# Optimization experiments

Hardware: AMD Instinct MI355X
Metric: run time of the kernel (lower is better)

## Reference

```python
import jax, jax.numpy as jnp
import numpy as np

THR = 1.0   # snntorch Leaky default threshold
BETA = 0.9  # leak factor from the module


@jax.custom_vjp
def atan_spike(x):
    # Heaviside forward; ATan surrogate gradient (snntorch default alpha=2):
    # d/dx = 1 / (1 + (pi * x)^2)
    return (x > 0).astype(x.dtype)

def _atan_fwd(x):
    return (x > 0).astype(x.dtype), x

def _atan_bwd(x, g):
    return (g / (1.0 + (jnp.pi * x) ** 2),)

atan_spike.defvjp(_atan_fwd, _atan_bwd)


def setup_inputs() -> dict:
    key = jax.random.key(0)
    k0, k1, k2, k3, k4 = jax.random.split(key, 5)
    B, T, L = 256, 1000, 30  # 24 = L - 7 + 1 matches fc1 in_features 16*24
    out_c = 35
    x = jax.random.normal(k0, (B, T, L), dtype=jnp.float32)
    conv_w = jax.random.normal(k1, (16, 1, 7), dtype=jnp.float32) / np.float32(np.sqrt(7.0))
    conv_b = jax.random.normal(k2, (16,), dtype=jnp.float32) * 0.05
    fc_w = jax.random.normal(k3, (out_c, 16 * 24), dtype=jnp.float32) / np.float32(np.sqrt(384.0))
    fc_b = jax.random.normal(k4, (out_c,), dtype=jnp.float32) * 0.05
    return {"x": x, "conv_w": conv_w, "conv_b": conv_b, "fc_w": fc_w, "fc_b": fc_b}


def reference(x, conv_w, conv_b, fc_w, fc_b):
    B, T, L = x.shape
    # Conv1d has no recurrence -> hoist it out of the time loop, batched over B*T.
    cur1 = jax.lax.conv_general_dilated(
        x.reshape(B * T, 1, L), conv_w, window_strides=(1,), padding="VALID",
        dimension_numbers=("NCH", "OIH", "NCH"),
    ) + conv_b[None, :, None]                      # (B*T, 16, 24)
    Lo = cur1.shape[-1]
    cur1 = cur1.reshape(B, T, 16, Lo).transpose(1, 0, 2, 3)  # (T, B, 16, 24)
    out_c = fc_w.shape[0]

    def step(carry, c1):
        mem1, mem2 = carry
        # LIF1: reset-by-subtraction using detached spike of previous membrane
        r1 = jax.lax.stop_gradient((mem1 > THR).astype(mem1.dtype))
        mem1 = BETA * mem1 + c1 - r1 * THR
        spk1 = atan_spike(mem1 - THR)              # (B, 16, 24)
        c2 = spk1.reshape(B, 16 * Lo) @ fc_w.T + fc_b  # (B, out_c)
        # LIF2
        r2 = jax.lax.stop_gradient((mem2 > THR).astype(mem2.dtype))
        mem2 = BETA * mem2 + c2 - r2 * THR
        return (mem1, mem2), mem2

    init = (jnp.zeros((B, 16, Lo), x.dtype), jnp.zeros((B, out_c), x.dtype))
    _, mem2_rec = jax.lax.scan(step, init, cur1)   # (T, B, out_c)
    return mem2_rec.mean(axis=0)                   # (B, out_c)
```

## Files before the change

kernel.cpp:

```cpp
#include <hip/hip_runtime.h>

typedef _Float16 half8 __attribute__((ext_vector_type(8)));
typedef float f32x4 __attribute__((ext_vector_type(4)));

#define SPH  32
#define NIT  34
#define SPKW 392
#define XTW  36
#define C2W  48
#define TN   1000

__global__ __launch_bounds__(576, 1) void snn_fwd(
    const float* __restrict__ x,
    const float* __restrict__ conv_w,
    const float* __restrict__ conv_b,
    const float* __restrict__ fc_w,
    const float* __restrict__ fc_b,
    float* __restrict__ out)
{
    __shared__ __align__(16) _Float16 spk[2][SPH][SPKW];
    __shared__ __align__(16) float    xsT[2][30][XTW];
    __shared__ __align__(16) float    c2L[2][SPH][C2W];

    const int tid  = threadIdx.x;
    const int b    = blockIdx.x;
    const int wid  = tid >> 6;
    const int lane = tid & 63;

    const int ct    = tid;
    const int cpair = ct & 7;
    const int p     = ct >> 3;
    const int c0    = cpair * 2;
    float wk0[7], wk1[7];
    float cb0 = 0.f, cb1 = 0.f;
    if (wid < 3) {
#pragma unroll
        for (int k = 0; k < 7; ++k) {
            wk0[k] = conv_w[c0 * 7 + k];
            wk1[k] = conv_w[(c0 + 1) * 7 + k];
        }
        cb0 = conv_b[c0];
        cb1 = conv_b[c0 + 1];
    }

    const int g  = wid - 3;
    const int m  = g >> 1;
    const int tb = g & 1;
    const int nL = lane & 15;
    const int q  = lane >> 4;
    half8 A[12];
    if (wid >= 3) {
        const int o = m * 16 + nL;
#pragma unroll
        for (int kt = 0; kt < 12; ++kt) {
            half8 a;
#pragma unroll
            for (int j = 0; j < 8; ++j) {
                int Kp = kt * 32 + q * 8 + j;
                int Kc = Kp & 15;
                int Kq = Kp >> 4;
                a[j] = (o < 35) ? (_Float16)fc_w[o * 384 + Kc * 24 + Kq]
                                : (_Float16)0.f;
            }
            A[kt] = a;
        }
    }
    const float fcb = (wid == 3 && lane < 35) ? fc_b[lane] : 0.f;

    const int st = tid - 192;
    int fs[3], fl[3];
    if (wid >= 3) {
#pragma unroll
        for (int r = 0; r < 3; ++r) {
            int f = st + 384 * r;
            fs[r] = f / 30;
            fl[r] = f % 30;
        }
    }

    float m1a = 0.f, spa = 0.f;
    float m1b = 0.f, spb = 0.f;
    float mem2 = 0.f, accO = 0.f;
    float xr[3];

    const float* xb = x + (size_t)b * (TN * 30);

    if (wid >= 3) {
#pragma unroll
        for (int r = 0; r < 3; ++r) {
            int f = st + 384 * r;
            if (f < 960) xsT[0][fl[r]][fs[r]] = xb[f];
        }
#pragma unroll
        for (int r = 0; r < 3; ++r) {
            int f = st + 384 * r;
            xr[r] = (f < 960) ? xb[960 + f] : 0.f;
        }
    }
    __syncthreads();

#pragma unroll 1
    for (int ph = 0; ph < NIT; ++ph) {
        if (wid < 3) {
            if (ph < 32) {
                const float* xcol = &xsT[ph & 1][p][0];
                unsigned int* sdst =
                    (unsigned int*)&spk[ph & 1][0][p * 16 + c0];
#pragma unroll 2
                for (int s0 = 0; s0 < SPH; s0 += 4) {
                    f32x4 xv[7];
#pragma unroll
                    for (int k = 0; k < 7; ++k)
                        xv[k] = *(const f32x4*)(xcol + k * XTW + s0);
                    float ca[4], cc[4];
#pragma unroll
                    for (int dt = 0; dt < 4; ++dt) { ca[dt] = cb0; cc[dt] = cb1; }
#pragma unroll
                    for (int k = 0; k < 7; ++k) {
#pragma unroll
                        for (int dt = 0; dt < 4; ++dt) {
                            ca[dt] = fmaf(wk0[k], xv[k][dt], ca[dt]);
                            cc[dt] = fmaf(wk1[k], xv[k][dt], cc[dt]);
                        }
                    }
#pragma unroll
                    for (int dt = 0; dt < 4; ++dt) {
                        m1a = fmaf(0.9f, m1a, ca[dt] - spa);
                        spa = (m1a > 1.0f) ? 1.0f : 0.0f;
                        m1b = fmaf(0.9f, m1b, cc[dt] - spb);
                        spb = (m1b > 1.0f) ? 1.0f : 0.0f;
                        unsigned int pk = (m1a > 1.0f ? 0x00003C00u : 0u) |
                                          (m1b > 1.0f ? 0x3C000000u : 0u);
                        sdst[(s0 + dt) * (SPKW / 2)] = pk;
                    }
                }
            }
        } else {
            const bool ldg = (ph <= 29);
            float xn[3];
            if (ldg) {
                const float* src = xb + (size_t)(ph + 2) * (SPH * 30);
#pragma unroll
                for (int r = 0; r < 3; ++r) {
                    int f = st + 384 * r;
                    int t = (ph + 2) * SPH + fs[r];
                    xn[r] = (f < 960 && t < TN) ? src[f] : 0.f;
                }
            }
            if (ph >= 1 && ph <= 32) {
                const _Float16* sb = &spk[(ph - 1) & 1][0][0];
                half8 B[12];
#pragma unroll
                for (int kt = 0; kt < 12; ++kt)
                    B[kt] = *(const half8*)(sb + (tb * 16 + nL) * SPKW + kt * 32 + q * 8);
                f32x4 acc = {0.f, 0.f, 0.f, 0.f};
#pragma unroll
                for (int kt = 0; kt < 12; ++kt)
                    acc = __builtin_amdgcn_mfma_f32_16x16x32_f16(A[kt], B[kt], acc, 0, 0, 0);
                float* cd = &c2L[(ph - 1) & 1][0][0];
                *(f32x4*)(cd + (tb * 16 + nL) * C2W + m * 16 + q * 4) = acc;
            }
            if (wid == 3 && lane < 35 && ph >= 2) {
                const float* cs = &c2L[(ph - 2) & 1][0][0];
                float v[SPH];
#pragma unroll
                for (int j = 0; j < SPH; ++j) v[j] = cs[j * C2W + lane];
                const int tbase = (ph - 2) * SPH;
#pragma unroll
                for (int j = 0; j < SPH; ++j) {
                    float r2 = (mem2 > 1.0f) ? 1.0f : 0.0f;
                    mem2 = 0.9f * mem2 + (v[j] + fcb) - r2;
                    if (tbase + j < TN) accO += mem2;
                }
            }
            if (ph <= 30) {
                float* dst = &xsT[(ph + 1) & 1][0][0];
#pragma unroll
                for (int r = 0; r < 3; ++r) {
                    int f = st + 384 * r;
                    if (f < 960) dst[fl[r] * XTW + fs[r]] = xr[r];
                }
            }
            if (ldg) {
#pragma unroll
                for (int r = 0; r < 3; ++r) xr[r] = xn[r];
            }
        }
        __syncthreads();
    }

    if (wid == 3 && lane < 35) out[b * 35 + lane] = accO * (1.0f / (float)TN);
}

extern "C" void kernel_launch(void* const* d_in, const int* in_sizes, int n_in,
                              void* d_out, int out_size, void* d_ws, size_t ws_size,
                              hipStream_t stream) {
    const float* x      = (const float*)d_in[0];
    const float* conv_w = (const float*)d_in[1];
    const float* conv_b = (const float*)d_in[2];
    const float* fc_w   = (const float*)d_in[3];
    const float* fc_b   = (const float*)d_in[4];
    float* out          = (float*)d_out;

    snn_fwd<<<256, 576, 0, stream>>>(x, conv_w, conv_b, fc_w, fc_b, out);
}
```

Baseline: 150.2 us.

## Double the time-chunk per phase and move the LIF2 scan to a dedicated wave

Raises the time steps processed per pipeline phase from 32 to 64, which roughly halves the number of block-wide barriers and phases. The MFMA waves now each handle two 16-row tiles, and the serial LIF2 accumulation moves to a new tenth wave so it no longer sits on an MFMA wave's critical path. The conv loop now double-buffers its LDS reads of x. The cost is a larger block (640 threads), more registers and LDS per block, and a longer serial LIF2 scan in each phase.

```diff
diff --git a/kernel.cpp b/kernel.cpp
--- a/kernel.cpp
+++ b/kernel.cpp
@@ -3,14 +3,14 @@
 typedef _Float16 half8 __attribute__((ext_vector_type(8)));
 typedef float f32x4 __attribute__((ext_vector_type(4)));
 
-#define SPH  32
-#define NIT  34
+#define SPH  64
+#define NIT  18
 #define SPKW 392
-#define XTW  36
+#define XTW  68
 #define C2W  48
 #define TN   1000
 
-__global__ __launch_bounds__(576, 1) void snn_fwd(
+__global__ __launch_bounds__(640, 1) void snn_fwd(
     const float* __restrict__ x,
     const float* __restrict__ conv_w,
     const float* __restrict__ conv_b,
@@ -43,13 +43,13 @@
         cb1 = conv_b[c0 + 1];
     }
 
-    const int g  = wid - 3;
-    const int m  = g >> 1;
-    const int tb = g & 1;
-    const int nL = lane & 15;
-    const int q  = lane >> 4;
+    const int g   = wid - 3;
+    const int m   = g % 3;
+    const int tb0 = g / 3;
+    const int nL  = lane & 15;
+    const int q   = lane >> 4;
     half8 A[12];
-    if (wid >= 3) {
+    if (wid >= 3 && wid < 9) {
         const int o = m * 16 + nL;
 #pragma unroll
         for (int kt = 0; kt < 12; ++kt) {
@@ -65,13 +65,13 @@
             A[kt] = a;
         }
     }
-    const float fcb = (wid == 3 && lane < 35) ? fc_b[lane] : 0.f;
+    const float fcb = (wid == 9 && lane < 35) ? fc_b[lane] : 0.f;
 
     const int st = tid - 192;
-    int fs[3], fl[3];
-    if (wid >= 3) {
-#pragma unroll
-        for (int r = 0; r < 3; ++r) {
+    int fs[5], fl[5];
+    if (wid >= 3 && wid < 9) {
+#pragma unroll
+        for (int r = 0; r < 5; ++r) {
             int f = st + 384 * r;
             fs[r] = f / 30;
             fl[r] = f % 30;
@@ -81,20 +81,20 @@
     float m1a = 0.f, spa = 0.f;
     float m1b = 0.f, spb = 0.f;
     float mem2 = 0.f, accO = 0.f;
-    float xr[3];
+    float xr[5];
 
     const float* xb = x + (size_t)b * (TN * 30);
 
-    if (wid >= 3) {
-#pragma unroll
-        for (int r = 0; r < 3; ++r) {
+    if (wid >= 3 && wid < 9) {
+#pragma unroll
+        for (int r = 0; r < 5; ++r) {
             int f = st + 384 * r;
-            if (f < 960) xsT[0][fl[r]][fs[r]] = xb[f];
-        }
-#pragma unroll
-        for (int r = 0; r < 3; ++r) {
+            xsT[0][fl[r]][fs[r]] = xb[f];
+        }
+#pragma unroll
+        for (int r = 0; r < 5; ++r) {
             int f = st + 384 * r;
-            xr[r] = (f < 960) ? xb[960 + f] : 0.f;
+            xr[r] = xb[1920 + f];
         }
     }
     __syncthreads();
@@ -102,16 +102,12 @@
 #pragma unroll 1
     for (int ph = 0; ph < NIT; ++ph) {
         if (wid < 3) {
-            if (ph < 32) {
+            if (ph < 16) {
                 const float* xcol = &xsT[ph & 1][p][0];
                 unsigned int* sdst =
                     (unsigned int*)&spk[ph & 1][0][p * 16 + c0];
-#pragma unroll 2
-                for (int s0 = 0; s0 < SPH; s0 += 4) {
-                    f32x4 xv[7];
-#pragma unroll
-                    for (int k = 0; k < 7; ++k)
-                        xv[k] = *(const f32x4*)(xcol + k * XTW + s0);
+
+                auto conv4 = [&](const f32x4* bf, int sb) {
                     float ca[4], cc[4];
 #pragma unroll
                     for (int dt = 0; dt < 4; ++dt) { ca[dt] = cb0; cc[dt] = cb1; }
@@ -119,8 +115,8 @@
                     for (int k = 0; k < 7; ++k) {
 #pragma unroll
                         for (int dt = 0; dt < 4; ++dt) {
-                            ca[dt] = fmaf(wk0[k], xv[k][dt], ca[dt]);
-                            cc[dt] = fmaf(wk1[k], xv[k][dt], cc[dt]);
+                            ca[dt] = fmaf(wk0[k], bf[k][dt], ca[dt]);
+                            cc[dt] = fmaf(wk1[k], bf[k][dt], cc[dt]);
                         }
                     }
 #pragma unroll
@@ -131,65 +127,90 @@
                         spb = (m1b > 1.0f) ? 1.0f : 0.0f;
                         unsigned int pk = (m1a > 1.0f ? 0x00003C00u : 0u) |
                                           (m1b > 1.0f ? 0x3C000000u : 0u);
-                        sdst[(s0 + dt) * (SPKW / 2)] = pk;
+                        sdst[(sb + dt) * (SPKW / 2)] = pk;
                     }
-                }
-            }
-        } else {
-            const bool ldg = (ph <= 29);
-            float xn[3];
+                };
+
+                f32x4 bA[7], bB[7];
+#pragma unroll
+                for (int k = 0; k < 7; ++k)
+                    bA[k] = *(const f32x4*)(xcol + k * XTW);
+#pragma unroll 2
+                for (int blk = 0; blk < 16; blk += 2) {
+                    const int sB = (blk + 1) * 4;
+#pragma unroll
+                    for (int k = 0; k < 7; ++k)
+                        bB[k] = *(const f32x4*)(xcol + k * XTW + sB);
+                    conv4(bA, blk * 4);
+                    const int sA = (blk + 2 < 16) ? (blk + 2) * 4 : 60;
+#pragma unroll
+                    for (int k = 0; k < 7; ++k)
+                        bA[k] = *(const f32x4*)(xcol + k * XTW + sA);
+                    conv4(bB, sB);
+                }
+            }
+        } else if (wid < 9) {
+            const bool ldg = (ph <= 13);
+            float xn[5];
             if (ldg) {
                 const float* src = xb + (size_t)(ph + 2) * (SPH * 30);
 #pragma unroll
-                for (int r = 0; r < 3; ++r) {
+                for (int r = 0; r < 5; ++r) {
                     int f = st + 384 * r;
                     int t = (ph + 2) * SPH + fs[r];
-                    xn[r] = (f < 960 && t < TN) ? src[f] : 0.f;
-                }
-            }
-            if (ph >= 1 && ph <= 32) {
+                    xn[r] = (t < TN) ? src[f] : 0.f;
+                }
+            }
+            if (ph >= 1 && ph <= 16) {
                 const _Float16* sb = &spk[(ph - 1) & 1][0][0];
-                half8 B[12];
-#pragma unroll
-                for (int kt = 0; kt < 12; ++kt)
-                    B[kt] = *(const half8*)(sb + (tb * 16 + nL) * SPKW + kt * 32 + q * 8);
-                f32x4 acc = {0.f, 0.f, 0.f, 0.f};
-#pragma unroll
-                for (int kt = 0; kt < 12; ++kt)
-                    acc = __builtin_amdgcn_mfma_f32_16x16x32_f16(A[kt], B[kt], acc, 0, 0, 0);
                 float* cd = &c2L[(ph - 1) & 1][0][0];
-                *(f32x4*)(cd + (tb * 16 + nL) * C2W + m * 16 + q * 4) = acc;
-            }
-            if (wid == 3 && lane < 35 && ph >= 2) {
+#pragma unroll
+                for (int task = 0; task < 2; ++task) {
+                    const int tb = tb0 + task * 2;
+                    half8 B[12];
+#pragma unroll
+                    for (int kt = 0; kt < 12; ++kt)
+                        B[kt] = *(const half8*)(sb + (tb * 16 + nL) * SPKW + kt * 32 + q * 8);
+                    f32x4 acc = {0.f, 0.f, 0.f, 0.f};
+#pragma unroll
+                    for (int kt = 0; kt < 12; ++kt)
+                        acc = __builtin_amdgcn_mfma_f32_16x16x32_f16(A[kt], B[kt], acc, 0, 0, 0);
+                    *(f32x4*)(cd + (tb * 16 + nL) * C2W + m * 16 + q * 4) = acc;
+                }
+            }
+            if (ph <= 14) {
+                float* dst = &xsT[(ph + 1) & 1][0][0];
+#pragma unroll
+                for (int r = 0; r < 5; ++r)
+                    dst[fl[r] * XTW + fs[r]] = xr[r];
+            }
+            if (ldg) {
+#pragma unroll
+                for (int r = 0; r < 5; ++r) xr[r] = xn[r];
+            }
+        } else {
+            if (lane < 35 && ph >= 2) {
                 const float* cs = &c2L[(ph - 2) & 1][0][0];
-                float v[SPH];
-#pragma unroll
-                for (int j = 0; j < SPH; ++j) v[j] = cs[j * C2W + lane];
                 const int tbase = (ph - 2) * SPH;
 #pragma unroll
-                for (int j = 0; j < SPH; ++j) {
-                    float r2 = (mem2 > 1.0f) ? 1.0f : 0.0f;
-                    mem2 = 0.9f * mem2 + (v[j] + fcb) - r2;
-                    if (tbase + j < TN) accO += mem2;
-                }
-            }
-            if (ph <= 30) {
-                float* dst = &xsT[(ph + 1) & 1][0][0];
-#pragma unroll
-                for (int r = 0; r < 3; ++r) {
-                    int f = st + 384 * r;
-                    if (f < 960) dst[fl[r] * XTW + fs[r]] = xr[r];
-                }
-            }
-            if (ldg) {
-#pragma unroll
-                for (int r = 0; r < 3; ++r) xr[r] = xn[r];
+                for (int jc = 0; jc < SPH; jc += 16) {
+                    float v[16];
+#pragma unroll
+                    for (int u = 0; u < 16; ++u)
+                        v[u] = cs[(jc + u) * C2W + lane];
+#pragma unroll
+                    for (int u = 0; u < 16; ++u) {
+                        float r2 = (mem2 > 1.0f) ? 1.0f : 0.0f;
+                        mem2 = 0.9f * mem2 + (v[u] + fcb) - r2;
+                        if (tbase + jc + u < TN) accO += mem2;
+                    }
+                }
             }
         }
         __syncthreads();
     }
 
-    if (wid == 3 && lane < 35) out[b * 35 + lane] = accO * (1.0f / (float)TN);
+    if (wid == 9 && lane < 35) out[b * 35 + lane] = accO * (1.0f / (float)TN);
 }
 
 extern "C" void kernel_launch(void* const* d_in, const int* in_sizes, int n_in,
@@ -202,5 +223,5 @@
     const float* fc_b   = (const float*)d_in[4];
     float* out          = (float*)d_out;
 
-    snn_fwd<<<256, 576, 0, stream>>>(x, conv_w, conv_b, fc_w, fc_b, out);
+    snn_fwd<<<256, 640, 0, stream>>>(x, conv_w, conv_b, fc_w, fc_b, out);
 }
```

Result: slower. 163.8 us (+9.1%).
